# Kernel optimization log

Hardware: AMD Instinct MI355X
Metric: run time of the kernel (lower is better)

Reference implementation:

```python
import jax, jax.numpy as jnp
import numpy as np

IN_F = 4096
OUT_F = 4096
THRESH = 0.1

def setup_inputs() -> dict:
    key = jax.random.key(0)
    kx, kw = jax.random.split(key)
    x = jax.random.normal(kx, (4, 2048, IN_F), dtype=jnp.float32)
    weight = jax.random.normal(kw, (OUT_F, IN_F), dtype=jnp.float32) * 0.5
    bias = jnp.zeros((OUT_F,), dtype=jnp.float32)
    return {"x": x, "weight": weight, "bias": bias}

def reference(x, weight, bias):
    # ternary quantization: sign(w) where |w| > 0.1, else 0
    q = jnp.sign(weight) * (jnp.abs(weight) > THRESH).astype(weight.dtype)
    # straight-through estimator: forward uses q, gradient flows to weight
    w_ste = weight + jax.lax.stop_gradient(q - weight)
    # F.linear: x @ w_ste.T + bias
    return jnp.einsum('bsi,oi->bso', x, w_ste) + bias
```

## Files before the change

### kernel.cpp

```cpp
#include <hip/hip_runtime.h>
#include <cstdint>
#include <cstddef>

#define MDIM 8192
#define NDIM 4096
#define KDIM 4096
#define TERN_THRESH 0.1f

typedef unsigned short u16;
typedef __bf16 bf16x8 __attribute__((ext_vector_type(8)));
typedef float f32x4 __attribute__((ext_vector_type(4)));
typedef u16 u16x8 __attribute__((ext_vector_type(8)));


__device__ __forceinline__ u16 f2bf(float f) {
  unsigned u = __float_as_uint(f);
  u += 0x7FFFu + ((u >> 16) & 1u);
  return (u16)(u >> 16);
}

__device__ __forceinline__ u16 tern_bf16(float w) {
  return w > TERN_THRESH ? (u16)0x3F80u : (w < -TERN_THRESH ? (u16)0xBF80u : (u16)0u);
}

__device__ __forceinline__ void load_lds16(const u16* g, u16* s) {
  __builtin_amdgcn_global_load_lds(
      (__attribute__((address_space(1))) void*)(void*)(g),
      (__attribute__((address_space(3))) void*)(void*)(s),
      16, 0, 0);
}


#define XBLOCKS ((MDIM * (size_t)KDIM) / (8 * 256))
#define WBLOCKS ((NDIM * (size_t)KDIM) / (8 * 256))

__global__ __launch_bounds__(256) void cvt_kernel(const float* __restrict__ x,
                                                  u16* __restrict__ xb,
                                                  const float* __restrict__ w,
                                                  u16* __restrict__ qb) {
  size_t b = blockIdx.x;
  if (b < XBLOCKS) {
    size_t i = b * 256 + threadIdx.x;
    const f32x4* x4 = (const f32x4*)x;
    f32x4 a = __builtin_nontemporal_load(&x4[2 * i]);
    f32x4 c = __builtin_nontemporal_load(&x4[2 * i + 1]);
    u16x8 o;
    o[0] = f2bf(a[0]); o[1] = f2bf(a[1]); o[2] = f2bf(a[2]); o[3] = f2bf(a[3]);
    o[4] = f2bf(c[0]); o[5] = f2bf(c[1]); o[6] = f2bf(c[2]); o[7] = f2bf(c[3]);
    ((u16x8*)xb)[i] = o;
  } else {
    size_t i = (b - XBLOCKS) * 256 + threadIdx.x;
    const f32x4* w4 = (const f32x4*)w;
    f32x4 a = __builtin_nontemporal_load(&w4[2 * i]);
    f32x4 c = __builtin_nontemporal_load(&w4[2 * i + 1]);
    u16x8 o;
    o[0] = tern_bf16(a[0]); o[1] = tern_bf16(a[1]); o[2] = tern_bf16(a[2]); o[3] = tern_bf16(a[3]);
    o[4] = tern_bf16(c[0]); o[5] = tern_bf16(c[1]); o[6] = tern_bf16(c[2]); o[7] = tern_bf16(c[3]);
    ((u16x8*)qb)[i] = o;
  }
}


__global__ __launch_bounds__(256) void gemm_tern_kernel(
    const u16* __restrict__ Xb,
    const u16* __restrict__ Qb,
    const float* __restrict__ bias,
    float* __restrict__ C) {
  __shared__ __attribute__((aligned(16))) u16 As[128 * 64];
  __shared__ __attribute__((aligned(16))) u16 Bs[128 * 64];

  const int tid  = threadIdx.x;
  const int lane = tid & 63;
  const int wv   = tid >> 6;
  const int wm   = wv >> 1;
  const int wn   = wv & 1;
  const int quad = lane >> 4;
  const int l16  = lane & 15;

  const int rowBase = blockIdx.y * 128;
  const int colBase = blockIdx.x * 128;

  const u16* ga[4];
  const u16* gb[4];
  u16* sa[4];
  u16* sb[4];
#pragma unroll
  for (int j = 0; j < 4; ++j) {
    int c  = tid + j * 256;
    int r  = c >> 3;
    int kc = (c & 7) ^ (r & 7);
    ga[j] = Xb + (size_t)(rowBase + r) * KDIM + kc * 8;
    gb[j] = Qb + (size_t)(colBase + r) * KDIM + kc * 8;
    sa[j] = (u16*)As + c * 8;
    sb[j] = (u16*)Bs + c * 8;
  }

  const int s7    = l16 & 7;
  const int koff0 = (quad ^ s7) * 8;
  int aoff[4], boff[4];
#pragma unroll
  for (int i = 0; i < 4; ++i) {
    aoff[i] = (wm * 64 + i * 16 + l16) * 64;
    boff[i] = (wn * 64 + i * 16 + l16) * 64;
  }

  f32x4 acc[4][4] = {};

  for (int kb = 0; kb < KDIM; kb += 64) {
    __syncthreads();
#pragma unroll
    for (int j = 0; j < 4; ++j) {
      load_lds16(ga[j] + kb, sa[j]);
      load_lds16(gb[j] + kb, sb[j]);
    }
    __syncthreads();
#pragma unroll
    for (int kk = 0; kk < 2; ++kk) {
      const int ko = koff0 ^ (kk * 32);
      bf16x8 af[4], bfr[4];
#pragma unroll
      for (int i = 0; i < 4; ++i) {
        af[i]  = *(const bf16x8*)((const u16*)As + aoff[i] + ko);
        bfr[i] = *(const bf16x8*)((const u16*)Bs + boff[i] + ko);
      }
#pragma unroll
      for (int i = 0; i < 4; ++i) {
#pragma unroll
        for (int j = 0; j < 4; ++j) {
          acc[i][j] = __builtin_amdgcn_mfma_f32_16x16x32_bf16(af[i], bfr[j], acc[i][j], 0, 0, 0);
        }
      }
    }
  }

  float bv[4];
#pragma unroll
  for (int j = 0; j < 4; ++j) bv[j] = bias[colBase + wn * 64 + j * 16 + l16];

#pragma unroll
  for (int i = 0; i < 4; ++i) {
#pragma unroll
    for (int r = 0; r < 4; ++r) {
      int grow = rowBase + wm * 64 + i * 16 + quad * 4 + r;
      float* crow = C + (size_t)grow * NDIM + colBase + wn * 64 + l16;
#pragma unroll
      for (int j = 0; j < 4; ++j) {
        crow[j * 16] = acc[i][j][r] + bv[j];
      }
    }
  }
}


extern "C" void kernel_launch(void* const* d_in, const int* in_sizes, int n_in,
                              void* d_out, int out_size, void* d_ws, size_t ws_size,
                              hipStream_t stream) {
  const float* x    = (const float*)d_in[0];
  const float* w    = (const float*)d_in[1];
  const float* bias = (const float*)d_in[2];
  float* out = (float*)d_out;

  u16* xb = (u16*)d_ws;
  u16* qb = xb + (size_t)MDIM * KDIM;

  cvt_kernel<<<(unsigned)(XBLOCKS + WBLOCKS), 256, 0, stream>>>(x, xb, w, qb);

  dim3 grid(NDIM / 128, MDIM / 128);
  gemm_tern_kernel<<<grid, 256, 0, stream>>>(xb, qb, bias, out);
}
```

Before: 500.2 us.

## Restructure ternary GEMM into 256x256 tiles with double-buffered async LDS pipeline

Replaces the 128x128, 256-thread GEMM with a 256x256 tile, 512-thread kernel that double-buffers LDS and issues global-to-LDS loads for the next K tile between MFMA blocks. It uses explicit vmcnt waits, barriers and s_setprio around MFMA clusters, plus an XCD-aware block remap and a new LDS swizzle. The aim is to hide global load latency behind compute and raise data reuse per tile. The cost is a larger LDS footprint and more accumulator registers per thread, which could reduce occupancy or cause spills.

```diff
diff --git a/kernel.cpp b/kernel.cpp
--- a/kernel.cpp
+++ b/kernel.cpp
@@ -61,76 +61,141 @@
 }
 
 
-__global__ __launch_bounds__(256) void gemm_tern_kernel(
+#define NT (KDIM / 64)
+
+#define BARRIER() __builtin_amdgcn_s_barrier()
+#define FENCE()   asm volatile("" ::: "memory")
+#define VMCNT4()  asm volatile("s_waitcnt vmcnt(4)" ::: "memory")
+
+#define MFMA_BLK(I0)                                                         \
+  do {                                                                       \
+    _Pragma("unroll") for (int _i = 0; _i < 4; ++_i) {                       \
+      _Pragma("unroll") for (int _j = 0; _j < 4; ++_j) {                     \
+        acc[(I0) + _i][_j] = __builtin_amdgcn_mfma_f32_16x16x32_bf16(        \
+            af[_i], bf[_j], acc[(I0) + _i][_j], 0, 0, 0);                    \
+      }                                                                      \
+    }                                                                        \
+  } while (0)
+
+__global__ __launch_bounds__(512, 2) void gemm_tern_kernel(
     const u16* __restrict__ Xb,
     const u16* __restrict__ Qb,
     const float* __restrict__ bias,
     float* __restrict__ C) {
-  __shared__ __attribute__((aligned(16))) u16 As[128 * 64];
-  __shared__ __attribute__((aligned(16))) u16 Bs[128 * 64];
+  __shared__ __attribute__((aligned(16))) u16 As[4 * 8192];
+  __shared__ __attribute__((aligned(16))) u16 Bs[4 * 8192];
 
   const int tid  = threadIdx.x;
   const int lane = tid & 63;
   const int wv   = tid >> 6;
-  const int wm   = wv >> 1;
-  const int wn   = wv & 1;
+  const int wm   = wv >> 2;
+  const int wn   = wv & 3;
   const int quad = lane >> 4;
   const int l16  = lane & 15;
 
-  const int rowBase = blockIdx.y * 128;
-  const int colBase = blockIdx.x * 128;
-
-  const u16* ga[4];
-  const u16* gb[4];
-  u16* sa[4];
-  u16* sb[4];
+  const int orig    = blockIdx.y * 16 + blockIdx.x;
+  const int wg      = (orig & 7) * 64 + (orig >> 3);
+  const int rowBase = (wg >> 4) * 256;
+  const int colBase = (wg & 15) * 256;
+
+  const u16* gA[2];
+  const u16* gB[2];
+  int sOff[2];
+#pragma unroll
+  for (int j = 0; j < 2; ++j) {
+    int c  = j * 512 + tid;
+    int r  = c >> 2;
+    int qg = (c & 3) ^ ((r >> 1) & 3);
+    gA[j]   = Xb + (size_t)(rowBase + r) * KDIM + qg * 8;
+    gB[j]   = Qb + (size_t)(colBase + r) * KDIM + qg * 8;
+    sOff[j] = c * 8;
+  }
+
+#define STAGE_A(b, h, ko)                                                        \
+  do {                                                                           \
+    load_lds16(gA[0] + (ko) + (h) * 32, (u16*)As + ((b) * 2 + (h)) * 8192 + sOff[0]); \
+    load_lds16(gA[1] + (ko) + (h) * 32, (u16*)As + ((b) * 2 + (h)) * 8192 + sOff[1]); \
+  } while (0)
+#define STAGE_B(b, h, ko)                                                        \
+  do {                                                                           \
+    load_lds16(gB[0] + (ko) + (h) * 32, (u16*)Bs + ((b) * 2 + (h)) * 8192 + sOff[0]); \
+    load_lds16(gB[1] + (ko) + (h) * 32, (u16*)Bs + ((b) * 2 + (h)) * 8192 + sOff[1]); \
+  } while (0)
+
+  int ac[8], bc[4];
+#pragma unroll
+  for (int i = 0; i < 8; ++i) {
+    int r = wm * 128 + i * 16 + l16;
+    ac[i] = (r * 4 + (quad ^ ((r >> 1) & 3))) * 8;
+  }
 #pragma unroll
   for (int j = 0; j < 4; ++j) {
-    int c  = tid + j * 256;
-    int r  = c >> 3;
-    int kc = (c & 7) ^ (r & 7);
-    ga[j] = Xb + (size_t)(rowBase + r) * KDIM + kc * 8;
-    gb[j] = Qb + (size_t)(colBase + r) * KDIM + kc * 8;
-    sa[j] = (u16*)As + c * 8;
-    sb[j] = (u16*)Bs + c * 8;
-  }
-
-  const int s7    = l16 & 7;
-  const int koff0 = (quad ^ s7) * 8;
-  int aoff[4], boff[4];
-#pragma unroll
-  for (int i = 0; i < 4; ++i) {
-    aoff[i] = (wm * 64 + i * 16 + l16) * 64;
-    boff[i] = (wn * 64 + i * 16 + l16) * 64;
-  }
-
-  f32x4 acc[4][4] = {};
-
-  for (int kb = 0; kb < KDIM; kb += 64) {
-    __syncthreads();
-#pragma unroll
-    for (int j = 0; j < 4; ++j) {
-      load_lds16(ga[j] + kb, sa[j]);
-      load_lds16(gb[j] + kb, sb[j]);
-    }
-    __syncthreads();
-#pragma unroll
-    for (int kk = 0; kk < 2; ++kk) {
-      const int ko = koff0 ^ (kk * 32);
-      bf16x8 af[4], bfr[4];
-#pragma unroll
-      for (int i = 0; i < 4; ++i) {
-        af[i]  = *(const bf16x8*)((const u16*)As + aoff[i] + ko);
-        bfr[i] = *(const bf16x8*)((const u16*)Bs + boff[i] + ko);
-      }
-#pragma unroll
-      for (int i = 0; i < 4; ++i) {
-#pragma unroll
-        for (int j = 0; j < 4; ++j) {
-          acc[i][j] = __builtin_amdgcn_mfma_f32_16x16x32_bf16(af[i], bfr[j], acc[i][j], 0, 0, 0);
-        }
-      }
-    }
+    int r = wn * 64 + j * 16 + l16;
+    bc[j] = (r * 4 + (quad ^ ((r >> 1) & 3))) * 8;
+  }
+
+#define RD_A(d, i, b, kk) d = *(const bf16x8*)((const u16*)As + ((b) * 2 + (kk)) * 8192 + ac[i])
+#define RD_B(d, j, b, kk) d = *(const bf16x8*)((const u16*)Bs + ((b) * 2 + (kk)) * 8192 + bc[j])
+
+  f32x4 acc[8][4] = {};
+  bf16x8 af[4], bf[4];
+
+  STAGE_A(0, 0, 0);
+  STAGE_B(0, 0, 0);
+  STAGE_A(0, 1, 0);
+  STAGE_B(0, 1, 0);
+  VMCNT4();
+  BARRIER();
+  FENCE();
+
+  int cur = 0;
+  for (int t = 0; t < NT; ++t) {
+    const int nxt = cur ^ 1;
+    const int kn  = (t + 1 < NT) ? (t + 1) * 64 : 0;
+
+    RD_A(af[0], 0, cur, 0); RD_A(af[1], 1, cur, 0);
+    RD_A(af[2], 2, cur, 0); RD_A(af[3], 3, cur, 0);
+    RD_B(bf[0], 0, cur, 0); RD_B(bf[1], 1, cur, 0);
+    RD_B(bf[2], 2, cur, 0); RD_B(bf[3], 3, cur, 0);
+    STAGE_A(nxt, 0, kn);
+    BARRIER(); FENCE();
+    __builtin_amdgcn_s_setprio(1);
+    MFMA_BLK(0);
+    __builtin_amdgcn_s_setprio(0);
+    BARRIER(); FENCE();
+
+    RD_A(af[0], 4, cur, 0); RD_A(af[1], 5, cur, 0);
+    RD_A(af[2], 6, cur, 0); RD_A(af[3], 7, cur, 0);
+    STAGE_B(nxt, 0, kn);
+    BARRIER(); FENCE();
+    __builtin_amdgcn_s_setprio(1);
+    MFMA_BLK(4);
+    __builtin_amdgcn_s_setprio(0);
+    VMCNT4();
+    BARRIER(); FENCE();
+
+    RD_A(af[0], 0, cur, 1); RD_A(af[1], 1, cur, 1);
+    RD_A(af[2], 2, cur, 1); RD_A(af[3], 3, cur, 1);
+    RD_B(bf[0], 0, cur, 1); RD_B(bf[1], 1, cur, 1);
+    RD_B(bf[2], 2, cur, 1); RD_B(bf[3], 3, cur, 1);
+    STAGE_A(nxt, 1, kn);
+    BARRIER(); FENCE();
+    __builtin_amdgcn_s_setprio(1);
+    MFMA_BLK(0);
+    __builtin_amdgcn_s_setprio(0);
+    BARRIER(); FENCE();
+
+    RD_A(af[0], 4, cur, 1); RD_A(af[1], 5, cur, 1);
+    RD_A(af[2], 6, cur, 1); RD_A(af[3], 7, cur, 1);
+    STAGE_B(nxt, 1, kn);
+    BARRIER(); FENCE();
+    __builtin_amdgcn_s_setprio(1);
+    MFMA_BLK(4);
+    __builtin_amdgcn_s_setprio(0);
+    VMCNT4();
+    BARRIER(); FENCE();
+
+    cur = nxt;
   }
 
   float bv[4];
@@ -138,10 +203,10 @@
   for (int j = 0; j < 4; ++j) bv[j] = bias[colBase + wn * 64 + j * 16 + l16];
 
 #pragma unroll
-  for (int i = 0; i < 4; ++i) {
+  for (int i = 0; i < 8; ++i) {
 #pragma unroll
     for (int r = 0; r < 4; ++r) {
-      int grow = rowBase + wm * 64 + i * 16 + quad * 4 + r;
+      int grow = rowBase + wm * 128 + i * 16 + quad * 4 + r;
       float* crow = C + (size_t)grow * NDIM + colBase + wn * 64 + l16;
 #pragma unroll
       for (int j = 0; j < 4; ++j) {
@@ -165,6 +230,6 @@
 
   cvt_kernel<<<(unsigned)(XBLOCKS + WBLOCKS), 256, 0, stream>>>(x, xb, w, qb);
 
-  dim3 grid(NDIM / 128, MDIM / 128);
-  gemm_tern_kernel<<<grid, 256, 0, stream>>>(xb, qb, bias, out);
-}
+  dim3 grid(NDIM / 256, MDIM / 256);
+  gemm_tern_kernel<<<grid, 512, 0, stream>>>(xb, qb, bias, out);
+}
```

New measurement: 497.6 us. No clear change (-0.5%).
